# Kernel tuning notes

Hardware: AMD Instinct MI355X
Metric: run time of the kernel (lower is better)

## Reference

```python
import jax, jax.numpy as jnp
import numpy as np

HEADS = 8
DIM_HEAD = 64
EPS = 1e-6


def _layernorm(t, w, b):
    # LayerNorm over last dim (dim_head), eps=1e-6, affine
    mu = jnp.mean(t, axis=-1, keepdims=True)
    var = jnp.mean((t - mu) ** 2, axis=-1, keepdims=True)
    return (t - mu) * jax.lax.rsqrt(var + EPS) * w + b


def setup_inputs() -> dict:
    key = jax.random.key(0)
    ks = jax.random.split(key, 8)
    B, N, DIM = 2, 32768, 512
    G = 32
    inner = HEADS * DIM_HEAD
    x = jax.random.normal(ks[0], (B, N, DIM), dtype=jnp.float32)
    batch = jnp.sort(jax.random.randint(ks[1], (N,), 0, G)).astype(jnp.int32)
    w_qkv = jax.random.normal(ks[2], (3 * inner, DIM), dtype=jnp.float32) * 0.02
    ln1_w = jnp.ones((DIM_HEAD,), jnp.float32)
    ln1_b = jnp.zeros((DIM_HEAD,), jnp.float32)
    ln2_w = jnp.ones((DIM_HEAD,), jnp.float32)
    ln2_b = jnp.zeros((DIM_HEAD,), jnp.float32)
    w_out = jax.random.normal(ks[3], (DIM, inner), dtype=jnp.float32) * 0.02
    b_out = jnp.zeros((DIM,), jnp.float32)
    return {
        "x": x, "w_qkv": w_qkv,
        "ln1_w": ln1_w, "ln1_b": ln1_b, "ln2_w": ln2_w, "ln2_b": ln2_b,
        "w_out": w_out, "b_out": b_out,
        "batch": batch, "num_graphs": G,
    }


def reference(x, w_qkv, ln1_w, ln1_b, ln2_w, ln2_b, w_out, b_out, batch, num_graphs):
    B, N, DIM = x.shape
    h, d = HEADS, DIM_HEAD
    inner = h * d
    qkv = x @ w_qkv.T  # [B, N, 3*inner]
    q, k, v = jnp.split(qkv, 3, axis=-1)
    # b n (h d) -> b h n d
    to_bhnd = lambda t: t.reshape(B, N, h, d).transpose(0, 2, 1, 3)
    q, k, v = to_bhnd(q), to_bhnd(k), to_bhnd(v)
    k = _layernorm(k, ln1_w, ln1_b)
    v = _layernorm(v, ln2_w, ln2_b)

    # segment structure: one-hot [G, N] over sorted graph ids
    onehot = (batch[None, :] == jnp.arange(num_graphs)[:, None]).astype(x.dtype)
    sizes = onehot.sum(axis=1)                      # [G] graph node counts
    qn = q / sizes[batch][None, None, :, None]      # q_i / size(graph(i))

    # sequential over graphs (fixed small G); per-graph k^T v then q @ ktv,
    # accumulated in place to avoid a [G,B,h,N,d] stack.
    def body(acc, mask):
        m = mask[None, None, :, None]
        ktv = jnp.einsum('bhnd,bhne->bhde', k * m, v)     # [B,h,d,d]
        og = jnp.einsum('bhnd,bhde->bhne', qn * m, ktv)   # [B,h,N,d]
        return acc + og, None

    out, _ = jax.lax.scan(body, jnp.zeros_like(qn), onehot)
    # b h n d -> b n (h d)
    out = out.transpose(0, 2, 1, 3).reshape(B, N, inner)
    return out @ w_out.T + b_out
```

## Files before the change

kernel.cpp:

```cpp
#include <hip/hip_runtime.h>
#include <hip/hip_bf16.h>
#include <stdint.h>

#define BATCH 2
#define NN 32768
#define DIM 512
#define HEADS 8
#define INNER 512
#define G 32
#define M_ROWS (BATCH * NN)
#define MAXCHUNK 576

typedef __attribute__((ext_vector_type(8))) short bf16x8;
typedef __attribute__((ext_vector_type(4))) float floatx4;

__device__ __forceinline__ void gl_lds16(const void* g, void* l) {
    __builtin_amdgcn_global_load_lds(
        (const __attribute__((address_space(1))) uint32_t*)g,
        (__attribute__((address_space(3))) uint32_t*)l, 16, 0, 0);
}

__device__ __forceinline__ short f2bs(float f) {
    __hip_bfloat16 h = __float2bfloat16(f);
    return *reinterpret_cast<short*>(&h);
}

__device__ __forceinline__ int xcd_swizzle(int bid, int nb) {
    return (bid & 7) * (nb >> 3) + (bid >> 3);
}

__device__ __forceinline__ bf16x8 frag_ld(const char* base, int r, int quad) {
    return *reinterpret_cast<const bf16x8*>(base + r * 64 + ((quad ^ ((r >> 1) & 3)) << 4));
}

__global__ void graph_info_kernel(const int* __restrict__ batch,
                                  int* __restrict__ starts,
                                  int* __restrict__ sizes,
                                  float* __restrict__ inv,
                                  int* __restrict__ crow0,
                                  int* __restrict__ crows,
                                  int* __restrict__ cbg,
                                  int* __restrict__ cnt) {
    __shared__ int bound[G + 1];
    int g = threadIdx.x;
    if (g <= G) {
        int lo = 0, hi = NN;
        while (lo < hi) { int mid = (lo + hi) >> 1; if (batch[mid] < g) lo = mid + 1; else hi = mid; }
        bound[g] = lo;
    }
    __syncthreads();
    if (g < G) {
        int s0 = bound[g], s1 = bound[g + 1];
        starts[g] = s0;
        int c = s1 - s0;
        sizes[g] = c;
        inv[g] = c ? 1.0f / (float)c : 0.0f;
    }
    if (g == 0) {
        int c = 0;
        for (int b = 0; b < BATCH; b++)
            for (int gg = 0; gg < G; gg++) {
                int s = bound[gg], sz = bound[gg + 1] - s;
                for (int i = 0; i < sz; i += 128) {
                    crow0[c] = b * NN + s + i;
                    crows[c] = min(128, sz - i);
                    cbg[c]   = b * G + gg;
                    c++;
                }
            }
        *cnt = c;
    }
}

__global__ __launch_bounds__(256) void convert_kernel(
        const float* __restrict__ in, __hip_bfloat16* __restrict__ out, int n8) {
    int i = blockIdx.x * 256 + threadIdx.x;
    if (i >= n8) return;
    const float4* p = reinterpret_cast<const float4*>(in) + (size_t)i * 2;
    float4 a = p[0], b = p[1];
    __hip_bfloat16 o[8];
    o[0] = __float2bfloat16(a.x); o[1] = __float2bfloat16(a.y);
    o[2] = __float2bfloat16(a.z); o[3] = __float2bfloat16(a.w);
    o[4] = __float2bfloat16(b.x); o[5] = __float2bfloat16(b.y);
    o[6] = __float2bfloat16(b.z); o[7] = __float2bfloat16(b.w);
    *reinterpret_cast<float4*>(out + (size_t)i * 8) = *reinterpret_cast<float4*>(o);
}

__global__ __launch_bounds__(256) void qkv_gemm_kernel(
        const __hip_bfloat16* __restrict__ xb, const __hip_bfloat16* __restrict__ wb,
        const float* __restrict__ ln1w, const float* __restrict__ ln1b,
        const float* __restrict__ ln2w, const float* __restrict__ ln2b,
        const float* __restrict__ inv, const int* __restrict__ batch,
        __hip_bfloat16* __restrict__ qn, __hip_bfloat16* __restrict__ kb,
        __hip_bfloat16* __restrict__ vb) {
    __shared__ alignas(16) char smem[32768];
    int bid = xcd_swizzle(blockIdx.y * 12 + blockIdx.x, 12 * 512);
    const int row0 = (bid / 12) * 128;
    const int col0 = (bid % 12) * 128;
    const int t = threadIdx.x;
    const int lane = t & 63;
    const int wave = t >> 6;
    const int wr = wave >> 1, wc = wave & 1;
    const int quad = lane >> 4, lr = lane & 15;

    floatx4 acc[4][4] = {};

    const int srow = t >> 2;
    const int scol = (((t & 3) ^ ((t >> 3) & 3))) * 8;
    const __hip_bfloat16* gA = xb + (size_t)(row0 + srow) * DIM + scol;
    const __hip_bfloat16* gB = wb + (size_t)(col0 + srow) * DIM + scol;
    char* lA = smem + t * 16;
    char* lB = smem + 8192 + t * 16;

    for (int k0 = 0; k0 < DIM; k0 += 32) {
        gl_lds16(gA + k0, lA);
        gl_lds16(gA + (size_t)64 * DIM + k0, lA + 4096);
        gl_lds16(gB + k0, lB);
        gl_lds16(gB + (size_t)64 * DIM + k0, lB + 4096);
        __syncthreads();
        bf16x8 af[4], bf[4];
        #pragma unroll
        for (int mt = 0; mt < 4; mt++)
            af[mt] = frag_ld(smem, wr * 64 + mt * 16 + lr, quad);
        #pragma unroll
        for (int nt = 0; nt < 4; nt++)
            bf[nt] = frag_ld(smem + 8192, wc * 64 + nt * 16 + lr, quad);
        #pragma unroll
        for (int mt = 0; mt < 4; mt++)
            #pragma unroll
            for (int nt = 0; nt < 4; nt++)
                acc[mt][nt] = __builtin_amdgcn_mfma_f32_16x16x32_bf16(af[mt], bf[nt], acc[mt][nt], 0, 0, 0);
        __syncthreads();
    }

    const int sel = (col0 + wc * 64) >> 9;
    const int hh = ((col0 + wc * 64) & 511) >> 6;

    if (sel == 0) {
        #pragma unroll
        for (int mt = 0; mt < 4; mt++) {
            #pragma unroll
            for (int reg = 0; reg < 4; reg++) {
                int row = row0 + wr * 64 + mt * 16 + quad * 4 + reg;
                int b_ = row >> 15;
                int n = row & (NN - 1);
                float s = inv[batch[n]];
                float v0 = acc[mt][0][reg] * s, v1 = acc[mt][1][reg] * s,
                      v2 = acc[mt][2][reg] * s, v3 = acc[mt][3][reg] * s;
                size_t base = ((size_t)b_ * NN + n) * INNER + hh * 64;
                qn[base + 0 * 16 + lr] = __float2bfloat16(v0);
                qn[base + 1 * 16 + lr] = __float2bfloat16(v1);
                qn[base + 2 * 16 + lr] = __float2bfloat16(v2);
                qn[base + 3 * 16 + lr] = __float2bfloat16(v3);
            }
        }
    } else {
        const float* w  = (sel == 1) ? ln1w : ln2w;
        const float* bb = (sel == 1) ? ln1b : ln2b;
        float lw[4], lb[4];
        #pragma unroll
        for (int nt = 0; nt < 4; nt++) { lw[nt] = w[nt * 16 + lr]; lb[nt] = bb[nt * 16 + lr]; }
        __hip_bfloat16* dstkv = (sel == 1) ? kb : vb;
        short* T = (short*)smem;

        #pragma unroll
        for (int mt = 0; mt < 4; mt++) {
            float f[4][4];
            #pragma unroll
            for (int reg = 0; reg < 4; reg++) {
                float v0 = acc[mt][0][reg], v1 = acc[mt][1][reg],
                      v2 = acc[mt][2][reg], v3 = acc[mt][3][reg];
                float s = v0 + v1 + v2 + v3;
                s += __shfl_xor(s, 1); s += __shfl_xor(s, 2);
                s += __shfl_xor(s, 4); s += __shfl_xor(s, 8);
                float mu = s * (1.0f / 64.0f);
                float d0 = v0 - mu, d1 = v1 - mu, d2 = v2 - mu, d3 = v3 - mu;
                float s2 = d0 * d0 + d1 * d1 + d2 * d2 + d3 * d3;
                s2 += __shfl_xor(s2, 1); s2 += __shfl_xor(s2, 2);
                s2 += __shfl_xor(s2, 4); s2 += __shfl_xor(s2, 8);
                float rstd = rsqrtf(s2 * (1.0f / 64.0f) + 1e-6f);
                f[reg][0] = d0 * rstd * lw[0] + lb[0];
                f[reg][1] = d1 * rstd * lw[1] + lb[1];
                f[reg][2] = d2 * rstd * lw[2] + lb[2];
                f[reg][3] = d3 * rstd * lw[3] + lb[3];
            }
            const int c0 = wr * 64 + mt * 16 + quad * 4;
            #pragma unroll
            for (int nt = 0; nt < 4; nt++) {
                int r = wc * 64 + nt * 16 + lr;
                int idx = r * 128 + (((c0 >> 3) ^ (r & 15)) << 3) + (c0 & 7);
                short4 pk;
                pk.x = f2bs(f[0][nt]); pk.y = f2bs(f[1][nt]);
                pk.z = f2bs(f[2][nt]); pk.w = f2bs(f[3][nt]);
                *reinterpret_cast<short4*>(&T[idx]) = pk;
            }
        }
        __syncthreads();
        const int b_ = row0 >> 15;
        const int n0 = row0 & (NN - 1);
        const int gidx = lane & 15;
        const int rbase = wave * 32 + (lane >> 4) * 8;
        short* dsts = (short*)dstkv;
        #pragma unroll
        for (int i = 0; i < 8; i++) {
            int r = rbase + i;
            int idx = r * 128 + ((gidx ^ (r & 15)) << 3);
            bf16x8 val = *reinterpret_cast<const bf16x8*>(&T[idx]);
            int j = (col0 & 511) + r;
            size_t addr = ((size_t)((b_ * HEADS + (j >> 6)) * 64 + (j & 63))) * NN
                          + n0 + gidx * 8;
            *reinterpret_cast<bf16x8*>(&dsts[addr]) = val;
        }
    }
}

__global__ __launch_bounds__(256) void ktv_w2_kernel(
        const short* __restrict__ kt, const short* __restrict__ vt,
        const short* __restrict__ wob,
        const int* __restrict__ starts, const int* __restrict__ sizes,
        short* __restrict__ w2t) {
    __shared__ alignas(16) float red[4][64][68];
    __shared__ alignas(16) short kt_sh[64][72];
    const int bhg = blockIdx.x;
    const int g = bhg & 31;
    const int bh = bhg >> 5;
    const int b = bh >> 3;
    const int h = bh & 7;
    const int s0 = starts[g];
    const int sz = sizes[g];
    const int t = threadIdx.x;
    const int lane = t & 63;
    const int w = t >> 6;
    const int quad = lane >> 4, lr = lane & 15;

    const int n0 = s0 & ~31;
    const int n1 = s0 + sz;
    const size_t base_bh = (size_t)bh * 64 * NN;

    const short* kp[4];
    const short* vp[4];
    #pragma unroll
    for (int mt = 0; mt < 4; mt++) {
        kp[mt] = kt + base_bh + (size_t)(mt * 16 + lr) * NN + quad * 8;
        vp[mt] = vt + base_bh + (size_t)(mt * 16 + lr) * NN + quad * 8;
    }

    floatx4 acc[4][4] = {};
    for (int c = n0 + w * 32; c < n1; c += 128) {
        bf16x8 af[4], bfr[4];
        if (c >= s0 && c + 32 <= n1) {
            #pragma unroll
            for (int mt = 0; mt < 4; mt++) {
                af[mt]  = *reinterpret_cast<const bf16x8*>(kp[mt] + c);
                bfr[mt] = *reinterpret_cast<const bf16x8*>(vp[mt] + c);
            }
        } else {
            #pragma unroll
            for (int mt = 0; mt < 4; mt++)
                #pragma unroll
                for (int j = 0; j < 8; j++) {
                    int n = c + quad * 8 + j;
                    bool ok = (n >= s0) && (n < n1);
                    af[mt][j]  = ok ? kp[mt][c + j] : (short)0;
                    bfr[mt][j] = ok ? vp[mt][c + j] : (short)0;
                }
        }
        #pragma unroll
        for (int mt = 0; mt < 4; mt++)
            #pragma unroll
            for (int et = 0; et < 4; et++)
                acc[mt][et] = __builtin_amdgcn_mfma_f32_16x16x32_bf16(af[mt], bfr[et], acc[mt][et], 0, 0, 0);
    }

    #pragma unroll
    for (int mt = 0; mt < 4; mt++)
        #pragma unroll
        for (int et = 0; et < 4; et++)
            *reinterpret_cast<floatx4*>(&red[w][lane][(mt * 4 + et) * 4]) = acc[mt][et];
    __syncthreads();
    {
        const int mt = w;
        #pragma unroll
        for (int et = 0; et < 4; et++) {
            floatx4 s = *reinterpret_cast<const floatx4*>(&red[0][lane][(mt * 4 + et) * 4]);
            #pragma unroll
            for (int w2 = 1; w2 < 4; w2++)
                s += *reinterpret_cast<const floatx4*>(&red[w2][lane][(mt * 4 + et) * 4]);
            #pragma unroll
            for (int reg = 0; reg < 4; reg++)
                kt_sh[mt * 16 + quad * 4 + reg][et * 16 + lr] = f2bs(s[reg]);
        }
    }
    __syncthreads();

    const short* wsl = wob + h * 64;
    short* w2 = w2t + (size_t)(b * G + g) * 512 * 512 + h * 64;
    bf16x8 b0[4], b1[4];
    #pragma unroll
    for (int dt = 0; dt < 4; dt++) {
        b0[dt] = *reinterpret_cast<const bf16x8*>(&kt_sh[dt * 16 + lr][quad * 8]);
        b1[dt] = *reinterpret_cast<const bf16x8*>(&kt_sh[dt * 16 + lr][quad * 8 + 32]);
    }
    for (int ct = 0; ct < 8; ct++) {
        int c = w * 128 + ct * 16 + lr;
        bf16x8 a0 = *reinterpret_cast<const bf16x8*>(wsl + (size_t)c * INNER + quad * 8);
        bf16x8 a1 = *reinterpret_cast<const bf16x8*>(wsl + (size_t)c * INNER + 32 + quad * 8);
        #pragma unroll
        for (int dt = 0; dt < 4; dt++) {
            floatx4 d = {0.f, 0.f, 0.f, 0.f};
            d = __builtin_amdgcn_mfma_f32_16x16x32_bf16(a0, b0[dt], d, 0, 0, 0);
            d = __builtin_amdgcn_mfma_f32_16x16x32_bf16(a1, b1[dt], d, 0, 0, 0);
            #pragma unroll
            for (int reg = 0; reg < 4; reg++) {
                int crow = w * 128 + ct * 16 + quad * 4 + reg;
                w2[(size_t)crow * 512 + dt * 16 + lr] = f2bs(d[reg]);
            }
        }
    }
}

__global__ __launch_bounds__(256) void final_gemm_kernel(
        const __hip_bfloat16* __restrict__ qn, const __hip_bfloat16* __restrict__ w2t,
        const float* __restrict__ bias,
        const int* __restrict__ crow0, const int* __restrict__ crows,
        const int* __restrict__ cbg, const int* __restrict__ cnt,
        float* __restrict__ out) {
    __shared__ alignas(16) char smem[16384];
    int bid = xcd_swizzle(blockIdx.y * 4 + blockIdx.x, 4 * MAXCHUNK);
    const int chunk = bid >> 2;
    if (chunk >= *cnt) return;
    const int row0  = crow0[chunk];
    const int nrows = crows[chunk];
    const int bg    = cbg[chunk];
    const int col0 = (bid & 3) * 128;
    const int t = threadIdx.x;
    const int lane = t & 63;
    const int wave = t >> 6;
    const int wr = wave >> 1, wc = wave & 1;
    const int quad = lane >> 4, lr = lane & 15;

    floatx4 acc[4][4] = {};

    const int srow = t >> 2;
    const int scol = (((t & 3) ^ ((t >> 3) & 3))) * 8;
    const __hip_bfloat16* gA = qn + (size_t)(row0 + srow) * INNER + scol;
    const __hip_bfloat16* gB = w2t + (size_t)bg * 512 * 512 + (size_t)(col0 + srow) * 512 + scol;
    char* lA = smem + t * 16;
    char* lB = smem + 8192 + t * 16;

    for (int k0 = 0; k0 < INNER; k0 += 32) {
        gl_lds16(gA + k0, lA);
        gl_lds16(gA + (size_t)64 * INNER + k0, lA + 4096);
        gl_lds16(gB + k0, lB);
        gl_lds16(gB + (size_t)64 * 512 + k0, lB + 4096);
        __syncthreads();
        bf16x8 af[4], bf[4];
        #pragma unroll
        for (int mt = 0; mt < 4; mt++)
            af[mt] = frag_ld(smem, wr * 64 + mt * 16 + lr, quad);
        #pragma unroll
        for (int nt = 0; nt < 4; nt++)
            bf[nt] = frag_ld(smem + 8192, wc * 64 + nt * 16 + lr, quad);
        #pragma unroll
        for (int mt = 0; mt < 4; mt++)
            #pragma unroll
            for (int nt = 0; nt < 4; nt++)
                acc[mt][nt] = __builtin_amdgcn_mfma_f32_16x16x32_bf16(af[mt], bf[nt], acc[mt][nt], 0, 0, 0);
        __syncthreads();
    }

    #pragma unroll
    for (int nt = 0; nt < 4; nt++) {
        int col = col0 + wc * 64 + nt * 16 + lr;
        float bv = bias[col];
        #pragma unroll
        for (int mt = 0; mt < 4; mt++)
            #pragma unroll
            for (int reg = 0; reg < 4; reg++) {
                int rl = wr * 64 + mt * 16 + quad * 4 + reg;
                if (rl < nrows)
                    out[(size_t)(row0 + rl) * DIM + col] = acc[mt][nt][reg] + bv;
            }
    }
}

extern "C" void kernel_launch(void* const* d_in, const int* in_sizes, int n_in,
                              void* d_out, int out_size, void* d_ws, size_t ws_size,
                              hipStream_t stream) {
    const float* x     = (const float*)d_in[0];
    const float* w_qkv = (const float*)d_in[1];
    const float* ln1w  = (const float*)d_in[2];
    const float* ln1b  = (const float*)d_in[3];
    const float* ln2w  = (const float*)d_in[4];
    const float* ln2b  = (const float*)d_in[5];
    const float* w_out = (const float*)d_in[6];
    const float* b_out = (const float*)d_in[7];
    const int*   batch = (const int*)d_in[8];
    float* out = (float*)d_out;

    char* ws = (char*)d_ws;
    const size_t MB = 1u << 20;
    __hip_bfloat16* qn  = (__hip_bfloat16*)(ws);
    __hip_bfloat16* kb  = (__hip_bfloat16*)(ws + 64 * MB);
    __hip_bfloat16* vb  = (__hip_bfloat16*)(ws + 128 * MB);
    __hip_bfloat16* xb  = (__hip_bfloat16*)(ws + 192 * MB);
    __hip_bfloat16* w2t = (__hip_bfloat16*)(ws + 192 * MB);
    __hip_bfloat16* wb  = (__hip_bfloat16*)(ws + 256 * MB);
    __hip_bfloat16* wob = (__hip_bfloat16*)(ws + 258 * MB);
    char* meta = ws + 259 * MB;
    int*   starts = (int*)(meta);
    int*   sizes  = (int*)(meta + 128);
    float* inv    = (float*)(meta + 256);
    int*   crow0  = (int*)(meta + 512);
    int*   crows  = (int*)(meta + 512 + 4096);
    int*   cbg    = (int*)(meta + 512 + 8192);
    int*   cnt    = (int*)(meta + 512 + 12288);

    graph_info_kernel<<<1, 64, 0, stream>>>(batch, starts, sizes, inv,
                                            crow0, crows, cbg, cnt);
    convert_kernel<<<(M_ROWS * DIM / 8 + 255) / 256, 256, 0, stream>>>(x, xb, M_ROWS * DIM / 8);
    convert_kernel<<<(3 * INNER * DIM / 8 + 255) / 256, 256, 0, stream>>>(w_qkv, wb, 3 * INNER * DIM / 8);
    convert_kernel<<<(DIM * INNER / 8 + 255) / 256, 256, 0, stream>>>(w_out, wob, DIM * INNER / 8);
    qkv_gemm_kernel<<<dim3((3 * INNER) / 128, M_ROWS / 128), 256, 0, stream>>>(
        xb, wb, ln1w, ln1b, ln2w, ln2b, inv, batch, qn, kb, vb);
    ktv_w2_kernel<<<BATCH * HEADS * G, 256, 0, stream>>>(
        (const short*)kb, (const short*)vb, (const short*)wob, starts, sizes, (short*)w2t);
    final_gemm_kernel<<<dim3(4, MAXCHUNK), 256, 0, stream>>>(
        qn, w2t, b_out, crow0, crows, cbg, cnt, out);
}
```

Baseline: 608.2 us.

## Double-buffer LDS in both GEMMs and merge the conversion launches

The QKV GEMM and the final grouped GEMM now use two LDS buffers. Each iteration issues the direct global-to-LDS loads for the next k-slice before computing on the current one, so one barrier per iteration is enough and load latency overlaps with MFMA work. Both kernels also get a launch-bounds hint to keep three blocks per CU. The three fp32-to-bf16 conversion launches are merged into one kernel that picks its source by block index, removing two launch overheads. The final GEMM's LDS doubles to 32 KB, which could limit occupancy or raise register pressure.

```diff
diff --git a/kernel.cpp b/kernel.cpp
--- a/kernel.cpp
+++ b/kernel.cpp
@@ -72,10 +72,18 @@
     }
 }
 
-__global__ __launch_bounds__(256) void convert_kernel(
-        const float* __restrict__ in, __hip_bfloat16* __restrict__ out, int n8) {
-    int i = blockIdx.x * 256 + threadIdx.x;
-    if (i >= n8) return;
+__global__ __launch_bounds__(256) void convert3_kernel(
+        const float* __restrict__ x, const float* __restrict__ wqkv,
+        const float* __restrict__ wout,
+        __hip_bfloat16* __restrict__ xb, __hip_bfloat16* __restrict__ wb,
+        __hip_bfloat16* __restrict__ wob) {
+    int blk = blockIdx.x;
+    const float* in;
+    __hip_bfloat16* out;
+    int i;
+    if (blk < 16384)      { in = x;    out = xb;  i = blk * 256 + threadIdx.x; }
+    else if (blk < 16768) { in = wqkv; out = wb;  i = (blk - 16384) * 256 + threadIdx.x; }
+    else                  { in = wout; out = wob; i = (blk - 16768) * 256 + threadIdx.x; }
     const float4* p = reinterpret_cast<const float4*>(in) + (size_t)i * 2;
     float4 a = p[0], b = p[1];
     __hip_bfloat16 o[8];
@@ -86,7 +94,7 @@
     *reinterpret_cast<float4*>(out + (size_t)i * 8) = *reinterpret_cast<float4*>(o);
 }
 
-__global__ __launch_bounds__(256) void qkv_gemm_kernel(
+__global__ __launch_bounds__(256, 3) void qkv_gemm_kernel(
         const __hip_bfloat16* __restrict__ xb, const __hip_bfloat16* __restrict__ wb,
         const float* __restrict__ ln1w, const float* __restrict__ ln1b,
         const float* __restrict__ ln2w, const float* __restrict__ ln2b,
@@ -112,19 +120,29 @@
     char* lA = smem + t * 16;
     char* lB = smem + 8192 + t * 16;
 
-    for (int k0 = 0; k0 < DIM; k0 += 32) {
-        gl_lds16(gA + k0, lA);
-        gl_lds16(gA + (size_t)64 * DIM + k0, lA + 4096);
-        gl_lds16(gB + k0, lB);
-        gl_lds16(gB + (size_t)64 * DIM + k0, lB + 4096);
-        __syncthreads();
+    gl_lds16(gA, lA);
+    gl_lds16(gA + (size_t)64 * DIM, lA + 4096);
+    gl_lds16(gB, lB);
+    gl_lds16(gB + (size_t)64 * DIM, lB + 4096);
+    __syncthreads();
+
+    for (int it = 0; it < DIM / 32; ++it) {
+        const int cb = (it & 1) << 14;
+        const int nb = cb ^ 16384;
+        const int k1 = (it + 1) * 32;
+        if (k1 < DIM) {
+            gl_lds16(gA + k1, lA + nb);
+            gl_lds16(gA + (size_t)64 * DIM + k1, lA + nb + 4096);
+            gl_lds16(gB + k1, lB + nb);
+            gl_lds16(gB + (size_t)64 * DIM + k1, lB + nb + 4096);
+        }
         bf16x8 af[4], bf[4];
         #pragma unroll
         for (int mt = 0; mt < 4; mt++)
-            af[mt] = frag_ld(smem, wr * 64 + mt * 16 + lr, quad);
+            af[mt] = frag_ld(smem + cb, wr * 64 + mt * 16 + lr, quad);
         #pragma unroll
         for (int nt = 0; nt < 4; nt++)
-            bf[nt] = frag_ld(smem + 8192, wc * 64 + nt * 16 + lr, quad);
+            bf[nt] = frag_ld(smem + cb + 8192, wc * 64 + nt * 16 + lr, quad);
         #pragma unroll
         for (int mt = 0; mt < 4; mt++)
             #pragma unroll
@@ -319,13 +337,13 @@
     }
 }
 
-__global__ __launch_bounds__(256) void final_gemm_kernel(
+__global__ __launch_bounds__(256, 3) void final_gemm_kernel(
         const __hip_bfloat16* __restrict__ qn, const __hip_bfloat16* __restrict__ w2t,
         const float* __restrict__ bias,
         const int* __restrict__ crow0, const int* __restrict__ crows,
         const int* __restrict__ cbg, const int* __restrict__ cnt,
         float* __restrict__ out) {
-    __shared__ alignas(16) char smem[16384];
+    __shared__ alignas(16) char smem[32768];
     int bid = xcd_swizzle(blockIdx.y * 4 + blockIdx.x, 4 * MAXCHUNK);
     const int chunk = bid >> 2;
     if (chunk >= *cnt) return;
@@ -348,19 +366,29 @@
     char* lA = smem + t * 16;
     char* lB = smem + 8192 + t * 16;
 
-    for (int k0 = 0; k0 < INNER; k0 += 32) {
-        gl_lds16(gA + k0, lA);
-        gl_lds16(gA + (size_t)64 * INNER + k0, lA + 4096);
-        gl_lds16(gB + k0, lB);
-        gl_lds16(gB + (size_t)64 * 512 + k0, lB + 4096);
-        __syncthreads();
+    gl_lds16(gA, lA);
+    gl_lds16(gA + (size_t)64 * INNER, lA + 4096);
+    gl_lds16(gB, lB);
+    gl_lds16(gB + (size_t)64 * 512, lB + 4096);
+    __syncthreads();
+
+    for (int it = 0; it < INNER / 32; ++it) {
+        const int cb = (it & 1) << 14;
+        const int nb = cb ^ 16384;
+        const int k1 = (it + 1) * 32;
+        if (k1 < INNER) {
+            gl_lds16(gA + k1, lA + nb);
+            gl_lds16(gA + (size_t)64 * INNER + k1, lA + nb + 4096);
+            gl_lds16(gB + k1, lB + nb);
+            gl_lds16(gB + (size_t)64 * 512 + k1, lB + nb + 4096);
+        }
         bf16x8 af[4], bf[4];
         #pragma unroll
         for (int mt = 0; mt < 4; mt++)
-            af[mt] = frag_ld(smem, wr * 64 + mt * 16 + lr, quad);
+            af[mt] = frag_ld(smem + cb, wr * 64 + mt * 16 + lr, quad);
         #pragma unroll
         for (int nt = 0; nt < 4; nt++)
-            bf[nt] = frag_ld(smem + 8192, wc * 64 + nt * 16 + lr, quad);
+            bf[nt] = frag_ld(smem + cb + 8192, wc * 64 + nt * 16 + lr, quad);
         #pragma unroll
         for (int mt = 0; mt < 4; mt++)
             #pragma unroll
@@ -418,9 +446,7 @@
 
     graph_info_kernel<<<1, 64, 0, stream>>>(batch, starts, sizes, inv,
                                             crow0, crows, cbg, cnt);
-    convert_kernel<<<(M_ROWS * DIM / 8 + 255) / 256, 256, 0, stream>>>(x, xb, M_ROWS * DIM / 8);
-    convert_kernel<<<(3 * INNER * DIM / 8 + 255) / 256, 256, 0, stream>>>(w_qkv, wb, 3 * INNER * DIM / 8);
-    convert_kernel<<<(DIM * INNER / 8 + 255) / 256, 256, 0, stream>>>(w_out, wob, DIM * INNER / 8);
+    convert3_kernel<<<16896, 256, 0, stream>>>(x, w_qkv, w_out, xb, wb, wob);
     qkv_gemm_kernel<<<dim3((3 * INNER) / 128, M_ROWS / 128), 256, 0, stream>>>(
         xb, wb, ln1w, ln1b, ln2w, ln2b, inv, batch, qn, kb, vb);
     ktv_w2_kernel<<<BATCH * HEADS * G, 256, 0, stream>>>(
```

Result: faster. 556.6 us (-8.5%).
